# Optimization experiments

Measured on AMD Instinct MI355X. Metric: run time of the kernel, lower is better.

## Reference

```python
import jax, jax.numpy as jnp
import numpy as np

IN_FEATURES = 4096
OUT_FEATURES = 11008
GROUP_SIZE = 128
GROUP_COUNT = 32


def _unpack_int4_first_dim(packed):
    # packed: [rows, cols] int32; each int32 holds 8 nibbles along dim 0
    shifts = jnp.arange(0, 32, 4, dtype=jnp.int32)  # [8]
    u = (packed[:, None, :] >> shifts[None, :, None]) & 15  # [rows, 8, cols]
    return u.reshape(packed.shape[0] * 8, packed.shape[1])


def _unpack_int4_last_dim(packed):
    shifts = jnp.arange(0, 32, 4, dtype=jnp.int32)  # [8]
    u = (packed[..., None] >> shifts) & 15  # [..., cols, 8]
    return u.reshape(*packed.shape[:-1], packed.shape[-1] * 8)


def setup_inputs() -> dict:
    key = jax.random.key(0)
    k1, k2, k3, k4 = jax.random.split(key, 4)
    x = jax.random.normal(k1, (4, 2048, IN_FEATURES), dtype=jnp.float32)
    qweight = jax.random.randint(k2, (IN_FEATURES // 8, OUT_FEATURES), 0, 2147483647, dtype=jnp.int32)
    qzeros = jax.random.randint(k3, (GROUP_COUNT, OUT_FEATURES // 8), 0, 2147483647, dtype=jnp.int32)
    # small positive per-group scales, as a real GPTQ checkpoint would have
    scales = (jax.random.uniform(k4, (GROUP_COUNT, OUT_FEATURES), dtype=jnp.float32) * 0.02 + 0.001).astype(jnp.float16)
    return {"x": x, "qweight": qweight, "qzeros": qzeros, "scales": scales}


def reference(x, qweight, qzeros, scales):
    # --- dequantize (fp32, as in _dequantize_autoround) ---
    weight_int = _unpack_int4_first_dim(qweight)[:IN_FEATURES, :OUT_FEATURES]  # [IN, OUT] int32
    s = scales.astype(jnp.float32)  # [G, OUT]
    group_ids = jnp.clip(jnp.arange(IN_FEATURES) // GROUP_SIZE, 0, GROUP_COUNT - 1)  # [IN]
    zeros = _unpack_int4_last_dim(qzeros)[:GROUP_COUNT, :OUT_FEATURES].astype(jnp.float32)  # [G, OUT]
    dequant = (weight_int.astype(jnp.float32) - zeros[group_ids]) * s[group_ids]  # [IN, OUT]
    # --- F.linear in compute_dtype fp16, cast back to x.dtype ---
    w16 = dequant.astype(jnp.float16)
    out = jnp.matmul(x.astype(jnp.float16), w16)  # [B, S, OUT]
    return out.astype(x.dtype)
```

## Files before the change

kernel.cpp:

```cpp
#include <hip/hip_runtime.h>
#include <hip/hip_fp16.h>


#define M_TOT 8192
#define N_TOT 11008
#define K_TOT 4096

typedef _Float16 half2v __attribute__((ext_vector_type(2)));
typedef _Float16 half8 __attribute__((ext_vector_type(8)));
typedef float float4v __attribute__((ext_vector_type(4)));

__global__ __launch_bounds__(256) void cvt_x_fp16(const float* __restrict__ x,
                                                  _Float16* __restrict__ a16) {
    const size_t i = ((size_t)blockIdx.x * 256 + threadIdx.x) * 8;
    float4v v0 = *(const float4v*)(x + i);
    float4v v1 = *(const float4v*)(x + i + 4);
    half8 h;
    h[0] = (_Float16)v0[0]; h[1] = (_Float16)v0[1];
    h[2] = (_Float16)v0[2]; h[3] = (_Float16)v0[3];
    h[4] = (_Float16)v1[0]; h[5] = (_Float16)v1[1];
    h[6] = (_Float16)v1[2]; h[7] = (_Float16)v1[3];
    *(half8*)(a16 + i) = h;
}

__global__ __launch_bounds__(256) void dequant_w(const int* __restrict__ qw,
                                                 const unsigned* __restrict__ qz,
                                                 const float* __restrict__ sc,
                                                 _Float16* __restrict__ wt) {
    const int tid = threadIdx.x;
    const int n = blockIdx.x * 32 + (tid >> 3);
    const int r = blockIdx.y * 8 + (tid & 7);
    const int g = r >> 4;
    const _Float16 s_h = (_Float16)sc[g * N_TOT + n];
    half2v sp; sp[0] = s_h; sp[1] = s_h;
    const unsigned zraw = qz[g * (N_TOT / 8) + (n >> 3)];
    const unsigned zn = (zraw >> ((n & 7) * 4)) & 15u;
    const half2v zp = __builtin_bit_cast(half2v, 0x64006400u | zn | (zn << 16));
    const unsigned raw = (unsigned)qw[(size_t)r * N_TOT + n];
    half8 w;
    #pragma unroll
    for (int p = 0; p < 4; ++p) {
        const unsigned bits = ((raw >> (4 * p)) & 0x000F000Fu) | 0x64006400u;
        half2v d = (__builtin_bit_cast(half2v, bits) - zp) * sp;
        w[p]     = d[0];
        w[p + 4] = d[1];
    }
    *(half8*)(wt + (size_t)n * K_TOT + r * 8) = w;
}

#define TBM 256
#define TBN 256
#define TBK 32
#define NKT (K_TOT / TBK)
#define TNBN (N_TOT / TBN)
#define TNBM (M_TOT / TBM)
#define TNWG (TNBN * TNBM)

__global__ __launch_bounds__(512, 2) void gemm_f16_8p(const _Float16* __restrict__ A,
                                                      const _Float16* __restrict__ B,
                                                      float* __restrict__ out) {
    __shared__ _Float16 As[4 * 256 * 32];
    __shared__ _Float16 Bs[4 * 256 * 32];

    const int tid = threadIdx.x;
    const int wave = tid >> 6;
    const int lane = tid & 63;

    const int flat = blockIdx.x;
    const int swz = (flat & 7) * (TNWG / 8) + (flat >> 3);
    const int n0 = (swz % TNBN) * TBN;
    const int m0 = (swz / TNBN) * TBM;

    const int wm = wave >> 2;
    const int wn = wave & 3;
    const int l16 = lane & 15;
    const int quad = lane >> 4;

    const int s_row  = wave * 16 + (lane >> 2);
    const int s_slot = ((lane & 3) ^ ((lane >> 2) & 3)) * 8;
    const _Float16* a_src = A + (size_t)(m0 + s_row) * K_TOT + s_slot;
    const _Float16* b_src = B + (size_t)(n0 + s_row) * K_TOT + s_slot;
    const int s_dst = wave * 512;

    const int rd_off = (quad ^ (l16 & 3)) * 8;

    #define STAGE_A(t) do {                                                      \
        const int b_ = (t) & 3;                                                  \
        const _Float16* s0_ = a_src + (size_t)(t) * TBK;                         \
        __builtin_amdgcn_global_load_lds(                                        \
            (const __attribute__((address_space(1))) void*)s0_,                  \
            (__attribute__((address_space(3))) void*)&As[b_ * 8192 + s_dst],     \
            16, 0, 0);                                                           \
        __builtin_amdgcn_global_load_lds(                                        \
            (const __attribute__((address_space(1))) void*)(s0_ + (size_t)128 * K_TOT), \
            (__attribute__((address_space(3))) void*)&As[b_ * 8192 + 4096 + s_dst],     \
            16, 0, 0);                                                           \
    } while (0)

    #define STAGE_B(t) do {                                                      \
        const int b_ = (t) & 3;                                                  \
        const _Float16* s0_ = b_src + (size_t)(t) * TBK;                         \
        __builtin_amdgcn_global_load_lds(                                        \
            (const __attribute__((address_space(1))) void*)s0_,                  \
            (__attribute__((address_space(3))) void*)&Bs[b_ * 8192 + s_dst],     \
            16, 0, 0);                                                           \
        __builtin_amdgcn_global_load_lds(                                        \
            (const __attribute__((address_space(1))) void*)(s0_ + (size_t)128 * K_TOT), \
            (__attribute__((address_space(3))) void*)&Bs[b_ * 8192 + 4096 + s_dst],     \
            16, 0, 0);                                                           \
    } while (0)

    float4v acc[8][4] = {};

    STAGE_A(0); STAGE_B(0);
    STAGE_A(1); STAGE_B(1);
    STAGE_A(2); STAGE_B(2);
    asm volatile("s_waitcnt vmcnt(8)" ::: "memory");
    __builtin_amdgcn_s_barrier();

    #define STEP(s, DO_STAGE, WAIT_STMT) do {                                    \
        const int b = (s) & 3;                                                   \
        const _Float16* Ab = &As[b * 8192];                                      \
        const _Float16* Bb = &Bs[b * 8192];                                      \
        half8 af[4], bf[4];                                                      \
                            \
        _Pragma("unroll")                                                        \
        for (int i = 0; i < 4; ++i)                                              \
            af[i] = *(const half8*)&Ab[(wm * 128 + i * 16 + l16) * TBK + rd_off];\
        _Pragma("unroll")                                                        \
        for (int j = 0; j < 4; ++j)                                              \
            bf[j] = *(const half8*)&Bb[(wn * 64 + j * 16 + l16) * TBK + rd_off]; \
        if (DO_STAGE) STAGE_A((s) + 3);                                          \
        __builtin_amdgcn_s_barrier();                                            \
        __builtin_amdgcn_s_setprio(1);                                           \
        _Pragma("unroll")                                                        \
        for (int i = 0; i < 4; ++i)                                              \
            _Pragma("unroll")                                                    \
            for (int j = 0; j < 4; ++j)                                          \
                acc[i][j] = __builtin_amdgcn_mfma_f32_16x16x32_f16(af[i], bf[j], acc[i][j], 0, 0, 0); \
        __builtin_amdgcn_s_setprio(0);                                           \
        __builtin_amdgcn_s_barrier();                                            \
                                     \
        _Pragma("unroll")                                                        \
        for (int i = 0; i < 4; ++i)                                              \
            af[i] = *(const half8*)&Ab[(wm * 128 + 64 + i * 16 + l16) * TBK + rd_off]; \
        if (DO_STAGE) STAGE_B((s) + 3);                                          \
        __builtin_amdgcn_s_barrier();                                            \
        __builtin_amdgcn_s_setprio(1);                                           \
        _Pragma("unroll")                                                        \
        for (int i = 0; i < 4; ++i)                                              \
            _Pragma("unroll")                                                    \
            for (int j = 0; j < 4; ++j)                                          \
                acc[4 + i][j] = __builtin_amdgcn_mfma_f32_16x16x32_f16(af[i], bf[j], acc[4 + i][j], 0, 0, 0); \
        __builtin_amdgcn_s_setprio(0);                                           \
        WAIT_STMT;                                                               \
        __builtin_amdgcn_s_barrier();                                            \
    } while (0)

    for (int s = 0; s < NKT - 3; ++s)
        STEP(s, 1, asm volatile("s_waitcnt vmcnt(8)" ::: "memory"));
    STEP(NKT - 3, 0, asm volatile("s_waitcnt vmcnt(4)" ::: "memory"));
    STEP(NKT - 2, 0, asm volatile("s_waitcnt vmcnt(0)" ::: "memory"));
    STEP(NKT - 1, 0, (void)0);

    #undef STEP
    #undef STAGE_A
    #undef STAGE_B

    float* o = out + (size_t)(m0 + wm * 128) * N_TOT + (n0 + wn * 64);
    #pragma unroll
    for (int mf = 0; mf < 8; ++mf)
        #pragma unroll
        for (int j = 0; j < 4; ++j)
            #pragma unroll
            for (int r = 0; r < 4; ++r)
                o[(size_t)(mf * 16 + quad * 4 + r) * N_TOT + (j * 16 + l16)] = acc[mf][j][r];
}

#define BM 128
#define BN 128
#define BK 64
#define LDK 72

__global__ __launch_bounds__(256) void gptq_fused_gemm(
    const float* __restrict__ x,
    const int* __restrict__ qw,
    const unsigned* __restrict__ qz,
    const float* __restrict__ sc,
    float* __restrict__ out)
{
    __shared__ _Float16 As[BM * LDK];
    __shared__ _Float16 Bs[BN * LDK];

    const int tid = threadIdx.x;
    const int m0 = blockIdx.y * BM;
    const int n0 = blockIdx.x * BN;

    const int wave = tid >> 6;
    const int lane = tid & 63;
    const int wr = wave >> 1;
    const int wc = wave & 1;
    const int l16 = lane & 15;
    const int quad = lane >> 4;

    const int a_k8 = tid & 7;
    const int a_m  = tid >> 3;
    const int b_n  = tid & 127;
    const int b_rr = tid >> 7;
    const int ncol = n0 + b_n;

    float4v acc[4][4] = {};

    for (int k0 = 0; k0 < K_TOT; k0 += BK) {
        __syncthreads();
        {
            const float* src = x + (size_t)(m0 + a_m) * K_TOT + k0 + a_k8 * 8;
            #pragma unroll
            for (int i = 0; i < 4; ++i) {
                const float* p = src + (size_t)(i * 32) * K_TOT;
                float4v v0 = *(const float4v*)p;
                float4v v1 = *(const float4v*)(p + 4);
                half8 h;
                h[0] = (_Float16)v0[0]; h[1] = (_Float16)v1[0];
                h[2] = (_Float16)v0[1]; h[3] = (_Float16)v1[1];
                h[4] = (_Float16)v0[2]; h[5] = (_Float16)v1[2];
                h[6] = (_Float16)v0[3]; h[7] = (_Float16)v1[3];
                *(half8*)&As[(a_m + 32 * i) * LDK + a_k8 * 8] = h;
            }
        }
        {
            const int g = k0 >> 7;
            const _Float16 s_h = (_Float16)sc[g * N_TOT + ncol];
            half2v sp; sp[0] = s_h; sp[1] = s_h;
            const unsigned zraw = qz[g * (N_TOT / 8) + (ncol >> 3)];
            const unsigned zn = (zraw >> ((ncol & 7) * 4)) & 15u;
            const half2v zp = __builtin_bit_cast(half2v, 0x64006400u | zn | (zn << 16));
            const int krow0 = k0 >> 3;
            #pragma unroll
            for (int i = 0; i < 4; ++i) {
                const int rr = b_rr + 2 * i;
                const unsigned raw = (unsigned)qw[(size_t)(krow0 + rr) * N_TOT + ncol];
                half8 w;
                #pragma unroll
                for (int p = 0; p < 4; ++p) {
                    const unsigned bits = ((raw >> (4 * p)) & 0x000F000Fu) | 0x64006400u;
                    half2v d = (__builtin_bit_cast(half2v, bits) - zp) * sp;
                    w[2 * p]     = d[0];
                    w[2 * p + 1] = d[1];
                }
                *(half8*)&Bs[b_n * LDK + rr * 8] = w;
            }
        }
        __syncthreads();
        #pragma unroll
        for (int kk = 0; kk < 2; ++kk) {
            half8 af[4], bf[4];
            #pragma unroll
            for (int i = 0; i < 4; ++i)
                af[i] = *(const half8*)&As[(wr * 64 + i * 16 + l16) * LDK + kk * 32 + quad * 8];
            #pragma unroll
            for (int j = 0; j < 4; ++j)
                bf[j] = *(const half8*)&Bs[(wc * 64 + j * 16 + l16) * LDK + kk * 32 + quad * 8];
            #pragma unroll
            for (int i = 0; i < 4; ++i)
                #pragma unroll
                for (int j = 0; j < 4; ++j)
                    acc[i][j] = __builtin_amdgcn_mfma_f32_16x16x32_f16(af[i], bf[j], acc[i][j], 0, 0, 0);
        }
    }

    float* o = out + (size_t)(m0 + wr * 64) * N_TOT + (n0 + wc * 64);
    #pragma unroll
    for (int i = 0; i < 4; ++i)
        #pragma unroll
        for (int j = 0; j < 4; ++j)
            #pragma unroll
            for (int r = 0; r < 4; ++r)
                o[(size_t)(i * 16 + quad * 4 + r) * N_TOT + (j * 16 + l16)] = acc[i][j][r];
}

extern "C" void kernel_launch(void* const* d_in, const int* in_sizes, int n_in,
                              void* d_out, int out_size, void* d_ws, size_t ws_size,
                              hipStream_t stream) {
    const float* x = (const float*)d_in[0];
    const int* qw = (const int*)d_in[1];
    const unsigned* qz = (const unsigned*)d_in[2];
    const float* sc = (const float*)d_in[3];
    float* out = (float*)d_out;

    const size_t a16_bytes = (size_t)M_TOT * K_TOT * 2;
    const size_t wt_bytes  = (size_t)N_TOT * K_TOT * 2;

    if (ws_size >= a16_bytes + wt_bytes) {
        _Float16* A16 = (_Float16*)d_ws;
        _Float16* Wt  = (_Float16*)((char*)d_ws + a16_bytes);
        cvt_x_fp16<<<dim3((M_TOT * K_TOT) / (256 * 8)), dim3(256), 0, stream>>>(x, A16);
        dequant_w<<<dim3(N_TOT / 32, 512 / 8), dim3(256), 0, stream>>>(qw, qz, sc, Wt);
        gemm_f16_8p<<<dim3(TNWG), dim3(512), 0, stream>>>(A16, Wt, out);
    } else {
        gptq_fused_gemm<<<dim3(N_TOT / BN, M_TOT / BM), dim3(256), 0, stream>>>(x, qw, qz, sc, out);
    }
}
```

Baseline: 1.225 ms.

## Software-pipeline LDS fragment loads across K steps and drop intra-step barriers

Splits the accumulators into two halves and prefetches the next K-step's A and B fragments from LDS at the end of each step, so LDS reads overlap MFMA work. Three of the four barriers per step are removed. The global-load wait is tightened from two stages in flight to one, so the prefetched buffer is guaranteed resident. This trades fewer synchronisations and better LDS/MFMA overlap for shallower global-memory latency hiding and higher register pressure.

```diff
diff --git a/kernel.cpp b/kernel.cpp
--- a/kernel.cpp
+++ b/kernel.cpp
@@ -56,7 +56,7 @@
 #define TNBM (M_TOT / TBM)
 #define TNWG (TNBN * TNBM)
 
-__global__ __launch_bounds__(512, 2) void gemm_f16_8p(const _Float16* __restrict__ A,
+__global__ __launch_bounds__(512, 2) void gemm_f16_pl(const _Float16* __restrict__ A,
                                                       const _Float16* __restrict__ B,
                                                       float* __restrict__ out) {
     __shared__ _Float16 As[4 * 256 * 32];
@@ -110,58 +110,67 @@
             16, 0, 0);                                                           \
     } while (0)
 
-    float4v acc[8][4] = {};
+    half8 af0[4], af1[4], bf[4];
+    float4v acc0[4][4] = {};
+    float4v acc1[4][4] = {};
 
     STAGE_A(0); STAGE_B(0);
     STAGE_A(1); STAGE_B(1);
     STAGE_A(2); STAGE_B(2);
-    asm volatile("s_waitcnt vmcnt(8)" ::: "memory");
+    asm volatile("s_waitcnt vmcnt(4)" ::: "memory");
     __builtin_amdgcn_s_barrier();
 
-    #define STEP(s, DO_STAGE, WAIT_STMT) do {                                    \
-        const int b = (s) & 3;                                                   \
-        const _Float16* Ab = &As[b * 8192];                                      \
-        const _Float16* Bb = &Bs[b * 8192];                                      \
-        half8 af[4], bf[4];                                                      \
-                            \
+    #pragma unroll
+    for (int i = 0; i < 4; ++i)
+        af0[i] = *(const half8*)&As[(wm * 128 + i * 16 + l16) * TBK + rd_off];
+    #pragma unroll
+    for (int j = 0; j < 4; ++j)
+        bf[j] = *(const half8*)&Bs[(wn * 64 + j * 16 + l16) * TBK + rd_off];
+
+    #define STEP(s, DO_STAGE, DO_PREFETCH, WAIT_STMT) do {                       \
+        const int cur = (s) & 3;                                                 \
+        const int nxt = ((s) + 1) & 3;                                           \
+        const _Float16* Ac = &As[cur * 8192];                                    \
+        const _Float16* An = &As[nxt * 8192];                                    \
+        const _Float16* Bn = &Bs[nxt * 8192];                                    \
+                \
         _Pragma("unroll")                                                        \
         for (int i = 0; i < 4; ++i)                                              \
-            af[i] = *(const half8*)&Ab[(wm * 128 + i * 16 + l16) * TBK + rd_off];\
-        _Pragma("unroll")                                                        \
-        for (int j = 0; j < 4; ++j)                                              \
-            bf[j] = *(const half8*)&Bb[(wn * 64 + j * 16 + l16) * TBK + rd_off]; \
+            af1[i] = *(const half8*)&Ac[(wm * 128 + 64 + i * 16 + l16) * TBK + rd_off]; \
         if (DO_STAGE) STAGE_A((s) + 3);                                          \
-        __builtin_amdgcn_s_barrier();                                            \
         __builtin_amdgcn_s_setprio(1);                                           \
         _Pragma("unroll")                                                        \
         for (int i = 0; i < 4; ++i)                                              \
             _Pragma("unroll")                                                    \
             for (int j = 0; j < 4; ++j)                                          \
-                acc[i][j] = __builtin_amdgcn_mfma_f32_16x16x32_f16(af[i], bf[j], acc[i][j], 0, 0, 0); \
+                acc0[i][j] = __builtin_amdgcn_mfma_f32_16x16x32_f16(af0[i], bf[j], acc0[i][j], 0, 0, 0); \
         __builtin_amdgcn_s_setprio(0);                                           \
-        __builtin_amdgcn_s_barrier();                                            \
-                                     \
-        _Pragma("unroll")                                                        \
-        for (int i = 0; i < 4; ++i)                                              \
-            af[i] = *(const half8*)&Ab[(wm * 128 + 64 + i * 16 + l16) * TBK + rd_off]; \
         if (DO_STAGE) STAGE_B((s) + 3);                                          \
-        __builtin_amdgcn_s_barrier();                                            \
         __builtin_amdgcn_s_setprio(1);                                           \
         _Pragma("unroll")                                                        \
         for (int i = 0; i < 4; ++i)                                              \
             _Pragma("unroll")                                                    \
             for (int j = 0; j < 4; ++j)                                          \
-                acc[4 + i][j] = __builtin_amdgcn_mfma_f32_16x16x32_f16(af[i], bf[j], acc[4 + i][j], 0, 0, 0); \
+                acc1[i][j] = __builtin_amdgcn_mfma_f32_16x16x32_f16(af1[i], bf[j], acc1[i][j], 0, 0, 0); \
         __builtin_amdgcn_s_setprio(0);                                           \
+         \
+        if (DO_PREFETCH) {                                                       \
+            _Pragma("unroll")                                                    \
+            for (int i = 0; i < 4; ++i)                                          \
+                af0[i] = *(const half8*)&An[(wm * 128 + i * 16 + l16) * TBK + rd_off]; \
+            _Pragma("unroll")                                                    \
+            for (int j = 0; j < 4; ++j)                                          \
+                bf[j] = *(const half8*)&Bn[(wn * 64 + j * 16 + l16) * TBK + rd_off];   \
+        }                                                                        \
         WAIT_STMT;                                                               \
         __builtin_amdgcn_s_barrier();                                            \
     } while (0)
 
     for (int s = 0; s < NKT - 3; ++s)
-        STEP(s, 1, asm volatile("s_waitcnt vmcnt(8)" ::: "memory"));
-    STEP(NKT - 3, 0, asm volatile("s_waitcnt vmcnt(4)" ::: "memory"));
-    STEP(NKT - 2, 0, asm volatile("s_waitcnt vmcnt(0)" ::: "memory"));
-    STEP(NKT - 1, 0, (void)0);
+        STEP(s, 1, 1, asm volatile("s_waitcnt vmcnt(4)" ::: "memory"));
+    STEP(NKT - 3, 0, 1, asm volatile("s_waitcnt vmcnt(0)" ::: "memory"));
+    STEP(NKT - 2, 0, 1, (void)0);
+    STEP(NKT - 1, 0, 0, (void)0);
 
     #undef STEP
     #undef STAGE_A
@@ -169,12 +178,14 @@
 
     float* o = out + (size_t)(m0 + wm * 128) * N_TOT + (n0 + wn * 64);
     #pragma unroll
-    for (int mf = 0; mf < 8; ++mf)
+    for (int i = 0; i < 4; ++i)
         #pragma unroll
         for (int j = 0; j < 4; ++j)
             #pragma unroll
-            for (int r = 0; r < 4; ++r)
-                o[(size_t)(mf * 16 + quad * 4 + r) * N_TOT + (j * 16 + l16)] = acc[mf][j][r];
+            for (int r = 0; r < 4; ++r) {
+                o[(size_t)(i * 16 + quad * 4 + r) * N_TOT + (j * 16 + l16)] = acc0[i][j][r];
+                o[(size_t)(64 + i * 16 + quad * 4 + r) * N_TOT + (j * 16 + l16)] = acc1[i][j][r];
+            }
 }
 
 #define BM 128
@@ -296,7 +307,7 @@
         _Float16* Wt  = (_Float16*)((char*)d_ws + a16_bytes);
         cvt_x_fp16<<<dim3((M_TOT * K_TOT) / (256 * 8)), dim3(256), 0, stream>>>(x, A16);
         dequant_w<<<dim3(N_TOT / 32, 512 / 8), dim3(256), 0, stream>>>(qw, qz, sc, Wt);
-        gemm_f16_8p<<<dim3(TNWG), dim3(512), 0, stream>>>(A16, Wt, out);
+        gemm_f16_pl<<<dim3(TNWG), dim3(512), 0, stream>>>(A16, Wt, out);
     } else {
         gptq_fused_gemm<<<dim3(N_TOT / BN, M_TOT / BM), dim3(256), 0, stream>>>(x, qw, qz, sc, out);
     }
```

New measurement: 1.224 ms. Within noise of the previous version (-0.1%).
